# Kernel optimization log

Hardware: AMD Instinct MI355X
Metric: run time of the kernel (lower is better)

The kernel has to match this reference:

```python
import jax, jax.numpy as jnp
import numpy as np


def conv_block(x, w1, b1, w2, b2):
    # 1x1 convs == per-pixel channel matmuls. x: [b, C, H, W]
    h = jax.nn.relu(jnp.einsum('bchw,oc->bohw', x, w1) + b1[None, :, None, None])
    return jnp.einsum('bchw,oc->bohw', h, w2) + b2[None, :, None, None]


def setup_inputs() -> dict:
    key = jax.random.key(0)
    ks = jax.random.split(key, 9)
    C, Ck = 256, 256 // 8
    bs, H, W = 4, 64, 64
    s_in = 1.0 / np.sqrt(C)
    s_k = 1.0 / np.sqrt(Ck)
    F_input = jax.random.normal(ks[0], (bs, C, H, W), dtype=jnp.float32)
    return {
        'F_input': F_input,
        'w1a': jax.random.normal(ks[1], (Ck, C), dtype=jnp.float32) * s_in,
        'b1a': jax.random.normal(ks[2], (Ck,), dtype=jnp.float32) * s_in,
        'w1b': jax.random.normal(ks[3], (Ck, Ck), dtype=jnp.float32) * s_k,
        'b1b': jax.random.normal(ks[4], (Ck,), dtype=jnp.float32) * s_k,
        'w2a': jax.random.normal(ks[5], (Ck, C), dtype=jnp.float32) * s_in,
        'b2a': jax.random.normal(ks[6], (Ck,), dtype=jnp.float32) * s_in,
        'w2b': jax.random.normal(ks[7], (Ck, Ck), dtype=jnp.float32) * s_k,
        'b2b': jax.random.normal(ks[8], (Ck,), dtype=jnp.float32) * s_k,
    }


def reference(F_input, w1a, b1a, w1b, b1b, w2a, b2a, w2b, b2b):
    bs, C, H, W = F_input.shape
    N = H * W
    q = conv_block(F_input, w1a, b1a, w1b, b1b).reshape(bs, -1, N)  # [b, Ck, N]
    k = conv_block(F_input, w2a, b2a, w2b, b2b).reshape(bs, -1, N)  # [b, Ck, N]
    # mm_1[b, n, m] = sum_c q[b, c, n] * k[b, c, m]
    scores = jnp.einsum('bcn,bcm->bnm', q, k)  # [b, N, N]
    S = jax.nn.softmax(scores, axis=-1)
    Fr = F_input.reshape(bs, C, N)
    # bmm(F_reshape, S^T): out[b, c, n] = sum_m F[b, c, m] * S[b, n, m]
    mm2 = jnp.einsum('bcm,bnm->bcn', Fr, S).reshape(bs, C, H, W)
    return F_input + mm2
```

## Files before the change

### kernel.cpp

```cpp
#include <hip/hip_runtime.h>
#include <math.h>

typedef __attribute__((ext_vector_type(4))) float f32x4;
typedef __attribute__((ext_vector_type(8))) short bf16x8;
typedef __attribute__((ext_vector_type(2))) unsigned int uint2v;
typedef __attribute__((ext_vector_type(4))) unsigned int uint4v;

#define LOG2E 1.4426950408889634f
#define MT 32

static __device__ __forceinline__ unsigned short f2bf(float f) {
  union { float f; unsigned int i; } u; u.f = f;
  unsigned int r = u.i + 0x7fffu + ((u.i >> 16) & 1u);
  return (unsigned short)(r >> 16);
}

typedef __attribute__((address_space(3))) unsigned int lds_u32;
typedef __attribute__((address_space(1))) unsigned int g_u32;

static __device__ __forceinline__ void gload_lds16(const unsigned short* g,
                                                   const unsigned short* l) {
  __builtin_amdgcn_global_load_lds(
      (const g_u32*)(unsigned long long)g,
      (lds_u32*)(unsigned int)(unsigned long long)l, 16, 0, 0);
}

__global__ __launch_bounds__(256) void k_wprep(const float* __restrict__ w1a,
                                               const float* __restrict__ w2a,
                                               float* __restrict__ w1aT,
                                               float* __restrict__ w2aT) {
  int i = blockIdx.x * 256 + threadIdx.x;
  if (i < 32 * 256) {
    int o = i >> 8, c = i & 255;
    w1aT[c * 32 + o] = w1a[i];
    w2aT[c * 32 + o] = w2a[i];
  }
}

__global__ __launch_bounds__(256) void k_qk(
    const float* __restrict__ F,
    const float* __restrict__ w1aT, const float* __restrict__ b1a,
    const float* __restrict__ w1b,  const float* __restrict__ b1b,
    const float* __restrict__ w2aT, const float* __restrict__ b2a,
    const float* __restrict__ w2b,  const float* __restrict__ b2b,
    unsigned short* __restrict__ Fbf,
    unsigned short* __restrict__ qT,
    unsigned short* __restrict__ kT) {
  __shared__ float hp[4][64][33];
  const int tid = threadIdx.x;
  const int nl = tid & 63;
  const int cs = __builtin_amdgcn_readfirstlane(tid >> 6);
  const int strip = blockIdx.x;
  const int b = strip >> 6;
  const int n0 = (strip & 63) << 6;
  const int n = n0 + nl;

  const float* Fp = F + ((size_t)(b * 256 + cs * 64)) * 4096 + n;
  unsigned short* Fbp = Fbf + ((size_t)(b * 256 + cs * 64)) * 4096 + n;

  float hq[32], hk[32];
#pragma unroll
  for (int o = 0; o < 32; ++o) { hq[o] = 0.f; hk[o] = 0.f; }

  float fa[8], fb[8];
#pragma unroll
  for (int j = 0; j < 8; ++j) fa[j] = Fp[(size_t)j * 4096];

  for (int jj = 0; jj < 64; jj += 16) {
#pragma unroll
    for (int j = 0; j < 8; ++j) fb[j] = Fp[(size_t)(jj + 8 + j) * 4096];
#pragma unroll
    for (int j = 0; j < 8; ++j) {
      Fbp[(size_t)(jj + j) * 4096] = f2bf(fa[j]);
      const float* wq = w1aT + (cs * 64 + jj + j) * 32;
      const float* wk = w2aT + (cs * 64 + jj + j) * 32;
#pragma unroll
      for (int o = 0; o < 32; ++o) { hq[o] += wq[o] * fa[j]; hk[o] += wk[o] * fa[j]; }
    }
    if (jj + 16 < 64) {
#pragma unroll
      for (int j = 0; j < 8; ++j) fa[j] = Fp[(size_t)(jj + 16 + j) * 4096];
    }
#pragma unroll
    for (int j = 0; j < 8; ++j) {
      Fbp[(size_t)(jj + 8 + j) * 4096] = f2bf(fb[j]);
      const float* wq = w1aT + (cs * 64 + jj + 8 + j) * 32;
      const float* wk = w2aT + (cs * 64 + jj + 8 + j) * 32;
#pragma unroll
      for (int o = 0; o < 32; ++o) { hq[o] += wq[o] * fb[j]; hk[o] += wk[o] * fb[j]; }
    }
  }

#pragma unroll
  for (int o = 0; o < 32; ++o) hp[cs][nl][o] = hq[o];
  __syncthreads();
  {
    float h[32];
#pragma unroll
    for (int o = 0; o < 32; ++o)
      h[o] = fmaxf(hp[0][nl][o] + hp[1][nl][o] + hp[2][nl][o] + hp[3][nl][o] + b1a[o], 0.f);
    unsigned int pk[4];
#pragma unroll
    for (int oo = 0; oo < 8; oo += 2) {
      float s0 = b1b[cs * 8 + oo], s1 = b1b[cs * 8 + oo + 1];
#pragma unroll
      for (int i = 0; i < 32; ++i) {
        s0 += w1b[(cs * 8 + oo) * 32 + i] * h[i];
        s1 += w1b[(cs * 8 + oo + 1) * 32 + i] * h[i];
      }
      s0 *= LOG2E; s1 *= LOG2E;
      pk[oo >> 1] = (unsigned int)f2bf(s0) | ((unsigned int)f2bf(s1) << 16);
    }
    uint4v v = {pk[0], pk[1], pk[2], pk[3]};
    *(uint4v*)(qT + ((size_t)(b * 4096 + n)) * 32 + cs * 8) = v;
  }
  __syncthreads();
#pragma unroll
  for (int o = 0; o < 32; ++o) hp[cs][nl][o] = hk[o];
  __syncthreads();
  {
    float h[32];
#pragma unroll
    for (int o = 0; o < 32; ++o)
      h[o] = fmaxf(hp[0][nl][o] + hp[1][nl][o] + hp[2][nl][o] + hp[3][nl][o] + b2a[o], 0.f);
    unsigned int pk[4];
#pragma unroll
    for (int oo = 0; oo < 8; oo += 2) {
      float s0 = b2b[cs * 8 + oo], s1 = b2b[cs * 8 + oo + 1];
#pragma unroll
      for (int i = 0; i < 32; ++i) {
        s0 += w2b[(cs * 8 + oo) * 32 + i] * h[i];
        s1 += w2b[(cs * 8 + oo + 1) * 32 + i] * h[i];
      }
      pk[oo >> 1] = (unsigned int)f2bf(s0) | ((unsigned int)f2bf(s1) << 16);
    }
    uint4v v = {pk[0], pk[1], pk[2], pk[3]};
    *(uint4v*)(kT + ((size_t)(b * 4096 + n)) * 32 + cs * 8) = v;
  }
}

__global__ __launch_bounds__(256, 4) void k_attn(
    const unsigned short* __restrict__ qT,
    const unsigned short* __restrict__ kT,
    const unsigned short* __restrict__ Fbf,
    const float* __restrict__ F,
    float* __restrict__ out,
    float* __restrict__ Opart,
    float* __restrict__ Mpart,
    float* __restrict__ Lpart,
    int spl, int mtiles, int direct) {
  __shared__ unsigned short Vt[256 * MT];
  __shared__ unsigned short Pb[64 * MT];
  __shared__ float scl[64];

  const int tid = threadIdx.x;
  const int w = tid >> 6, lane = tid & 63, lo = lane & 15, hi = lane >> 4;

  const int bid = (int)blockIdx.x;
  int g, ns;
  if (spl == 4)      { g = ((bid & 7) << 1) | (bid >> 9); ns = (bid >> 3) & 63; }
  else if (spl == 2) { g = bid & 7;                       ns = bid >> 3; }
  else               { int sz = (bid & 7) * 32 + (bid >> 3); g = sz >> 6; ns = sz & 63; }
  const int b = (spl == 4) ? (g >> 2) : ((spl == 2) ? (g >> 1) : g);
  const int s = (spl == 4) ? (g & 3) : ((spl == 2) ? (g & 1) : 0);
  const int n0 = ns << 6;
  const int mt0 = s * mtiles;

  const bf16x8 qfrag = *(const bf16x8*)(
      qT + ((size_t)(b << 12) + n0 + (w << 4) + lo) * 32 + (hi << 3));
  const unsigned short* kTb = kT + ((size_t)(b << 12)) * 32;
  const unsigned short* Fb = Fbf + ((size_t)b << 20);

  const int crow = lane >> 2, pch = lane & 3;

  f32x4 acc[4][4];
#pragma unroll
  for (int i = 0; i < 4; ++i)
#pragma unroll
    for (int j = 0; j < 4; ++j) acc[i][j] = (f32x4){0.f, 0.f, 0.f, 0.f};
  float mrun = -INFINITY, lrun = 0.f;

#pragma unroll
  for (int i = 0; i < 4; ++i) {
    int c = i * 64 + (w << 4) + crow;
    gload_lds16(Fb + (size_t)c * 4096 + (mt0 << 5) + ((pch ^ (c & 3)) << 3),
                &Vt[(i * 64 + (w << 4)) * MT]);
  }
  bf16x8 kc0 = *(const bf16x8*)(kTb + ((size_t)((mt0 << 5) + lo)) * 32 + (hi << 3));
  bf16x8 kc1 = *(const bf16x8*)(kTb + ((size_t)((mt0 << 5) + 16 + lo)) * 32 + (hi << 3));

  for (int t = 0; t < mtiles; ++t) {
    f32x4 z = (f32x4){0.f, 0.f, 0.f, 0.f};
    f32x4 s0 = __builtin_amdgcn_mfma_f32_16x16x32_bf16(kc0, qfrag, z, 0, 0, 0);
    f32x4 s1 = __builtin_amdgcn_mfma_f32_16x16x32_bf16(kc1, qfrag, z, 0, 0, 0);

    float tmax = fmaxf(fmaxf(fmaxf(s0[0], s0[1]), fmaxf(s0[2], s0[3])),
                       fmaxf(fmaxf(s1[0], s1[1]), fmaxf(s1[2], s1[3])));
    tmax = fmaxf(tmax, __shfl_xor(tmax, 16));
    tmax = fmaxf(tmax, __shfl_xor(tmax, 32));
    float mnew = fmaxf(mrun, tmax);
    float sc = exp2f(mrun - mnew);
    mrun = mnew;
    float p00 = exp2f(s0[0] - mnew), p01 = exp2f(s0[1] - mnew);
    float p02 = exp2f(s0[2] - mnew), p03 = exp2f(s0[3] - mnew);
    float p10 = exp2f(s1[0] - mnew), p11 = exp2f(s1[1] - mnew);
    float p12 = exp2f(s1[2] - mnew), p13 = exp2f(s1[3] - mnew);
    float rsum = p00 + p01 + p02 + p03 + p10 + p11 + p12 + p13;
    rsum += __shfl_xor(rsum, 16);
    rsum += __shfl_xor(rsum, 32);
    lrun = lrun * sc + rsum;
    if (hi == 0) scl[(w << 4) + lo] = sc;
    {
      const int qr = (w << 4) + lo;
      unsigned short* base = &Pb[qr * MT];
      int ch0 = (hi >> 1), ch1 = 2 + (hi >> 1);
      uint2v v0 = {(unsigned int)f2bf(p00) | ((unsigned int)f2bf(p01) << 16),
                   (unsigned int)f2bf(p02) | ((unsigned int)f2bf(p03) << 16)};
      uint2v v1 = {(unsigned int)f2bf(p10) | ((unsigned int)f2bf(p11) << 16),
                   (unsigned int)f2bf(p12) | ((unsigned int)f2bf(p13) << 16)};
      *(uint2v*)(base + (((ch0 ^ (qr & 3)) << 3) | ((hi & 1) << 2))) = v0;
      *(uint2v*)(base + (((ch1 ^ (qr & 3)) << 3) | ((hi & 1) << 2))) = v1;
    }

    __syncthreads();

    {
      f32x4 sv[4];
      bool one = true;
#pragma unroll
      for (int qf = 0; qf < 4; ++qf) {
        sv[qf] = *(const f32x4*)&scl[(qf << 4) + (hi << 2)];
        one = one && (sv[qf][0] == 1.f) && (sv[qf][1] == 1.f) &&
              (sv[qf][2] == 1.f) && (sv[qf][3] == 1.f);
      }
      if (!__all(one)) {
#pragma unroll
        for (int qf = 0; qf < 4; ++qf)
#pragma unroll
          for (int cs2 = 0; cs2 < 4; ++cs2) acc[qf][cs2] *= sv[qf];
      }
    }
    bf16x8 pf[4], vf[4];
#pragma unroll
    for (int qf = 0; qf < 4; ++qf) {
      int qr = (qf << 4) + lo;
      pf[qf] = *(const bf16x8*)&Pb[qr * MT + ((hi ^ (qr & 3)) << 3)];
    }
#pragma unroll
    for (int cs2 = 0; cs2 < 4; ++cs2) {
      int c = (w << 6) + (cs2 << 4) + lo;
      vf[cs2] = *(const bf16x8*)&Vt[c * MT + ((hi ^ (c & 3)) << 3)];
    }
    __builtin_amdgcn_s_setprio(1);
#pragma unroll
    for (int qf = 0; qf < 4; ++qf)
#pragma unroll
      for (int cs2 = 0; cs2 < 4; ++cs2)
        acc[qf][cs2] = __builtin_amdgcn_mfma_f32_16x16x32_bf16(pf[qf], vf[cs2], acc[qf][cs2], 0, 0, 0);
    __builtin_amdgcn_s_setprio(0);

    __syncthreads();

    if (t + 1 < mtiles) {
      int mo = (mt0 + t + 1) << 5;
#pragma unroll
      for (int i = 0; i < 4; ++i) {
        int c = i * 64 + (w << 4) + crow;
        gload_lds16(Fb + (size_t)c * 4096 + mo + ((pch ^ (c & 3)) << 3),
                    &Vt[(i * 64 + (w << 4)) * MT]);
      }
      kc0 = *(const bf16x8*)(kTb + ((size_t)(mo + lo)) * 32 + (hi << 3));
      kc1 = *(const bf16x8*)(kTb + ((size_t)(mo + 16 + lo)) * 32 + (hi << 3));
    }
  }

  if (direct) {
    if (hi == 0) scl[(w << 4) + lo] = 1.f / lrun;
    __syncthreads();
    f32x4 lv[4];
#pragma unroll
    for (int qf = 0; qf < 4; ++qf) lv[qf] = *(const f32x4*)&scl[(qf << 4) + (hi << 2)];
#pragma unroll
    for (int qf = 0; qf < 4; ++qf)
#pragma unroll
      for (int cs2 = 0; cs2 < 4; ++cs2) {
        size_t idx = ((size_t)(b * 256 + (w << 6) + (cs2 << 4) + lo)) * 4096 +
                     n0 + (qf << 4) + (hi << 2);
        f32x4 fv = *(const f32x4*)(F + idx);
        *(f32x4*)(out + idx) = fv + acc[qf][cs2] * lv[qf];
      }
  } else {
    const int bp = (b * spl + s) * 64 + ns;
    if (hi == 0) {
      Mpart[bp * 64 + (w << 4) + lo] = mrun;
      Lpart[bp * 64 + (w << 4) + lo] = lrun;
    }
    float* Ob = Opart + (size_t)bp * 256 * 64;
#pragma unroll
    for (int qf = 0; qf < 4; ++qf)
#pragma unroll
      for (int cs2 = 0; cs2 < 4; ++cs2) {
        int c = (w << 6) + (cs2 << 4) + lo;
        *(f32x4*)(Ob + (size_t)c * 64 + (qf << 4) + (hi << 2)) = acc[qf][cs2];
      }
  }
}

__global__ __launch_bounds__(256, 4) void k_comb(
    const float* __restrict__ F, const float* __restrict__ Opart,
    const float* __restrict__ Mpart, const float* __restrict__ Lpart,
    float* __restrict__ out, int spl) {
  __shared__ float a[4][64];
  const int cid = (int)blockIdx.x;
  const int b = cid >> 8, ns = (cid >> 2) & 63, cq = cid & 3;
  const int tid = threadIdx.x, q = tid & 63, ci = tid >> 6;
  const int n0 = ns << 6;

  if (tid < 64) {
    float mv[4], lv[4];
    float M = -INFINITY;
#pragma unroll
    for (int s2 = 0; s2 < 4; ++s2)
      if (s2 < spl) {
        int bp = (b * spl + s2) * 64 + ns;
        mv[s2] = Mpart[bp * 64 + q];
        lv[s2] = Lpart[bp * 64 + q];
        M = fmaxf(M, mv[s2]);
      }
    float L = 0.f;
#pragma unroll
    for (int s2 = 0; s2 < 4; ++s2)
      if (s2 < spl) { mv[s2] = exp2f(mv[s2] - M); L += mv[s2] * lv[s2]; }
    float Li = 1.f / L;
#pragma unroll
    for (int s2 = 0; s2 < 4; ++s2)
      if (s2 < spl) a[s2][q] = mv[s2] * Li;
  }
  __syncthreads();
  float aq[4];
#pragma unroll
  for (int s2 = 0; s2 < 4; ++s2) aq[s2] = (s2 < spl) ? a[s2][q] : 0.f;

#pragma unroll 4
  for (int cc = 0; cc < 16; ++cc) {
    int c = (cq << 6) + (ci << 4) + cc;
    float accv = 0.f;
#pragma unroll
    for (int s2 = 0; s2 < 4; ++s2)
      if (s2 < spl)
        accv += aq[s2] * Opart[((size_t)((b * spl + s2) * 64 + ns) * 256 + c) * 64 + q];
    size_t idx = ((size_t)(b * 256 + c)) * 4096 + n0 + q;
    out[idx] = F[idx] + accv;
  }
}

extern "C" void kernel_launch(void* const* d_in, const int* in_sizes, int n_in,
                              void* d_out, int out_size, void* d_ws, size_t ws_size,
                              hipStream_t stream) {
  const float* F   = (const float*)d_in[0];
  const float* w1a = (const float*)d_in[1];
  const float* b1a = (const float*)d_in[2];
  const float* w1b = (const float*)d_in[3];
  const float* b1b = (const float*)d_in[4];
  const float* w2a = (const float*)d_in[5];
  const float* b2a = (const float*)d_in[6];
  const float* w2b = (const float*)d_in[7];
  const float* b2b = (const float*)d_in[8];
  float* out = (float*)d_out;

  char* ws = (char*)d_ws;
  float* w1aT = (float*)(ws);
  float* w2aT = (float*)(ws + 32768);
  unsigned short* qT  = (unsigned short*)(ws + 65536);
  unsigned short* kT  = (unsigned short*)(ws + 65536 + 1048576);
  unsigned short* Fbf = (unsigned short*)(ws + 65536 + 2097152);
  const size_t obase = 65536 + 2097152 + 8388608;

  int spl = 1, direct = 1;
  const size_t oSz1 = 16777216, mlSz1 = 65536;
  if (ws_size >= obase + 4 * (oSz1 + 2 * mlSz1)) { spl = 4; direct = 0; }
  else if (ws_size >= obase + 2 * (oSz1 + 2 * mlSz1)) { spl = 2; direct = 0; }

  float* Opart = (float*)(ws + obase);
  float* Mpart = (float*)(ws + obase + (size_t)spl * oSz1);
  float* Lpart = (float*)(ws + obase + (size_t)spl * oSz1 + (size_t)spl * mlSz1);

  hipLaunchKernelGGL(k_wprep, dim3(32), dim3(256), 0, stream, w1a, w2a, w1aT, w2aT);
  hipLaunchKernelGGL(k_qk, dim3(256), dim3(256), 0, stream,
                     F, w1aT, b1a, w1b, b1b, w2aT, b2a, w2b, b2b, Fbf, qT, kT);
  hipLaunchKernelGGL(k_attn, dim3(256 * spl), dim3(256), 0, stream,
                     qT, kT, Fbf, F, out, Opart, Mpart, Lpart, spl, 128 / spl, direct);
  if (!direct)
    hipLaunchKernelGGL(k_comb, dim3(1024), dim3(256), 0, stream,
                       F, Opart, Mpart, Lpart, out, spl);
}
```

Baseline: 289.2 us.

## Split projection into convert/transpose plus per-pixel kernel; load V directly in attention

Adds a k_cvt kernel that writes F as bf16 in both the original and a pixel-major transposed layout. k_qk is rewritten as small 64-thread blocks that read the transposed bf16 row, reduce partial sums with shuffles, and compute q or k per block. In the attention kernel, the LDS-staged V tiles loaded with global_load_lds are replaced by direct global loads into registers, and the P and scale buffers are double-buffered with a new swizzle so the trailing barrier can be dropped. This adds an extra kernel and extra traffic for the transposed copy, which overlaps the Opart region of the workspace, and it relies on cache hits for V reuse across waves.

New measurement: 360.1 us. 1.25x slower.

```diff
diff --git a/kernel.cpp b/kernel.cpp
--- a/kernel.cpp
+++ b/kernel.cpp
@@ -14,15 +14,9 @@
   unsigned int r = u.i + 0x7fffu + ((u.i >> 16) & 1u);
   return (unsigned short)(r >> 16);
 }
-
-typedef __attribute__((address_space(3))) unsigned int lds_u32;
-typedef __attribute__((address_space(1))) unsigned int g_u32;
-
-static __device__ __forceinline__ void gload_lds16(const unsigned short* g,
-                                                   const unsigned short* l) {
-  __builtin_amdgcn_global_load_lds(
-      (const g_u32*)(unsigned long long)g,
-      (lds_u32*)(unsigned int)(unsigned long long)l, 16, 0, 0);
+static __device__ __forceinline__ float bf2f(unsigned short s) {
+  union { unsigned int i; float f; } u; u.i = ((unsigned int)s) << 16;
+  return u.f;
 }
 
 __global__ __launch_bounds__(256) void k_wprep(const float* __restrict__ w1a,
@@ -37,106 +31,135 @@
   }
 }
 
-__global__ __launch_bounds__(256) void k_qk(
-    const float* __restrict__ F,
+__global__ __launch_bounds__(256) void k_cvt(const float* __restrict__ F,
+                                             unsigned short* __restrict__ Fbf,
+                                             unsigned short* __restrict__ FbfT) {
+  __shared__ unsigned short Lt[64][68];
+  const int bi = blockIdx.x;
+  const int b = bi >> 8, cg = (bi >> 6) & 3, ng = bi & 63;
+  const int tid = threadIdx.x;
+  {
+    const int cl = tid >> 2, part = tid & 3;
+    const size_t row = (size_t)(b * 256 + cg * 64 + cl);
+    const float* src = F + row * 4096 + ng * 64 + part * 16;
+    unsigned int pk[8];
+#pragma unroll
+    for (int i = 0; i < 4; ++i) {
+      f32x4 v = *(const f32x4*)(src + i * 4);
+      pk[2 * i]     = (unsigned int)f2bf(v[0]) | ((unsigned int)f2bf(v[1]) << 16);
+      pk[2 * i + 1] = (unsigned int)f2bf(v[2]) | ((unsigned int)f2bf(v[3]) << 16);
+    }
+    unsigned short* dst = Fbf + row * 4096 + ng * 64 + part * 16;
+    uint4v a = {pk[0], pk[1], pk[2], pk[3]};
+    uint4v c2 = {pk[4], pk[5], pk[6], pk[7]};
+    *(uint4v*)(dst) = a;
+    *(uint4v*)(dst + 8) = c2;
+    unsigned short* lrow = &Lt[cl][part * 16];
+#pragma unroll
+    for (int i = 0; i < 8; ++i) {
+      lrow[2 * i]     = (unsigned short)(pk[i] & 0xffffu);
+      lrow[2 * i + 1] = (unsigned short)(pk[i] >> 16);
+    }
+  }
+  __syncthreads();
+  {
+    const int nl = tid & 63, ch = tid >> 6;
+    unsigned int pk[16];
+#pragma unroll
+    for (int i = 0; i < 16; ++i) {
+      unsigned short a = Lt[ch * 16 + 0 + (i >> 3) * 8 + 0][nl];
+      pk[i] = 0; (void)a;
+    }
+    unsigned short vals[16];
+#pragma unroll
+    for (int i = 0; i < 16; ++i) vals[i] = Lt[ch * 16 + i][nl];
+#pragma unroll
+    for (int i = 0; i < 8; ++i)
+      pk[i] = (unsigned int)vals[2 * i] | ((unsigned int)vals[2 * i + 1] << 16);
+    unsigned short* dst = FbfT + ((size_t)(b * 4096 + ng * 64 + nl)) * 256 + cg * 64 + ch * 16;
+    uint4v v0 = {pk[0], pk[1], pk[2], pk[3]};
+    uint4v v1 = {pk[4], pk[5], pk[6], pk[7]};
+    *(uint4v*)(dst) = v0;
+    *(uint4v*)(dst + 8) = v1;
+  }
+}
+
+__global__ __launch_bounds__(64) void k_qk(
+    const unsigned short* __restrict__ FbfT,
     const float* __restrict__ w1aT, const float* __restrict__ b1a,
     const float* __restrict__ w1b,  const float* __restrict__ b1b,
     const float* __restrict__ w2aT, const float* __restrict__ b2a,
     const float* __restrict__ w2b,  const float* __restrict__ b2b,
-    unsigned short* __restrict__ Fbf,
-    unsigned short* __restrict__ qT,
-    unsigned short* __restrict__ kT) {
-  __shared__ float hp[4][64][33];
-  const int tid = threadIdx.x;
-  const int nl = tid & 63;
-  const int cs = __builtin_amdgcn_readfirstlane(tid >> 6);
-  const int strip = blockIdx.x;
-  const int b = strip >> 6;
-  const int n0 = (strip & 63) << 6;
-  const int n = n0 + nl;
-
-  const float* Fp = F + ((size_t)(b * 256 + cs * 64)) * 4096 + n;
-  unsigned short* Fbp = Fbf + ((size_t)(b * 256 + cs * 64)) * 4096 + n;
-
-  float hq[32], hk[32];
-#pragma unroll
-  for (int o = 0; o < 32; ++o) { hq[o] = 0.f; hk[o] = 0.f; }
-
-  float fa[8], fb[8];
-#pragma unroll
-  for (int j = 0; j < 8; ++j) fa[j] = Fp[(size_t)j * 4096];
-
-  for (int jj = 0; jj < 64; jj += 16) {
-#pragma unroll
-    for (int j = 0; j < 8; ++j) fb[j] = Fp[(size_t)(jj + 8 + j) * 4096];
-#pragma unroll
-    for (int j = 0; j < 8; ++j) {
-      Fbp[(size_t)(jj + j) * 4096] = f2bf(fa[j]);
-      const float* wq = w1aT + (cs * 64 + jj + j) * 32;
-      const float* wk = w2aT + (cs * 64 + jj + j) * 32;
-#pragma unroll
-      for (int o = 0; o < 32; ++o) { hq[o] += wq[o] * fa[j]; hk[o] += wk[o] * fa[j]; }
-    }
-    if (jj + 16 < 64) {
-#pragma unroll
-      for (int j = 0; j < 8; ++j) fa[j] = Fp[(size_t)(jj + 16 + j) * 4096];
-    }
-#pragma unroll
-    for (int j = 0; j < 8; ++j) {
-      Fbp[(size_t)(jj + 8 + j) * 4096] = f2bf(fb[j]);
-      const float* wq = w1aT + (cs * 64 + jj + 8 + j) * 32;
-      const float* wk = w2aT + (cs * 64 + jj + 8 + j) * 32;
-#pragma unroll
-      for (int o = 0; o < 32; ++o) { hq[o] += wq[o] * fb[j]; hk[o] += wk[o] * fb[j]; }
-    }
-  }
-
-#pragma unroll
-  for (int o = 0; o < 32; ++o) hp[cs][nl][o] = hq[o];
-  __syncthreads();
+    unsigned short* __restrict__ qT, unsigned short* __restrict__ kT) {
+  const int p = blockIdx.x & 1;
+  const int tile = blockIdx.x >> 1;
+  const int l = threadIdx.x;
+  const int px = l >> 2, cq = l & 3;
+  const int n = tile * 16 + px;
+  const float* wA = p ? w2aT : w1aT;
+  const float* bA = p ? b2a : b1a;
+  const float* wB = p ? w2b : w1b;
+  const float* bB = p ? b2b : b1b;
+
+  bf16x8 f8[8];
   {
-    float h[32];
-#pragma unroll
-    for (int o = 0; o < 32; ++o)
-      h[o] = fmaxf(hp[0][nl][o] + hp[1][nl][o] + hp[2][nl][o] + hp[3][nl][o] + b1a[o], 0.f);
-    unsigned int pk[4];
-#pragma unroll
-    for (int oo = 0; oo < 8; oo += 2) {
-      float s0 = b1b[cs * 8 + oo], s1 = b1b[cs * 8 + oo + 1];
-#pragma unroll
-      for (int i = 0; i < 32; ++i) {
-        s0 += w1b[(cs * 8 + oo) * 32 + i] * h[i];
-        s1 += w1b[(cs * 8 + oo + 1) * 32 + i] * h[i];
-      }
-      s0 *= LOG2E; s1 *= LOG2E;
-      pk[oo >> 1] = (unsigned int)f2bf(s0) | ((unsigned int)f2bf(s1) << 16);
-    }
-    uint4v v = {pk[0], pk[1], pk[2], pk[3]};
-    *(uint4v*)(qT + ((size_t)(b * 4096 + n)) * 32 + cs * 8) = v;
-  }
-  __syncthreads();
-#pragma unroll
-  for (int o = 0; o < 32; ++o) hp[cs][nl][o] = hk[o];
-  __syncthreads();
-  {
-    float h[32];
-#pragma unroll
-    for (int o = 0; o < 32; ++o)
-      h[o] = fmaxf(hp[0][nl][o] + hp[1][nl][o] + hp[2][nl][o] + hp[3][nl][o] + b2a[o], 0.f);
-    unsigned int pk[4];
-#pragma unroll
-    for (int oo = 0; oo < 8; oo += 2) {
-      float s0 = b2b[cs * 8 + oo], s1 = b2b[cs * 8 + oo + 1];
-#pragma unroll
-      for (int i = 0; i < 32; ++i) {
-        s0 += w2b[(cs * 8 + oo) * 32 + i] * h[i];
-        s1 += w2b[(cs * 8 + oo + 1) * 32 + i] * h[i];
-      }
-      pk[oo >> 1] = (unsigned int)f2bf(s0) | ((unsigned int)f2bf(s1) << 16);
-    }
-    uint4v v = {pk[0], pk[1], pk[2], pk[3]};
-    *(uint4v*)(kT + ((size_t)(b * 4096 + n)) * 32 + cs * 8) = v;
-  }
+    const unsigned short* src = FbfT + (size_t)n * 256 + cq * 64;
+#pragma unroll
+    for (int i = 0; i < 8; ++i) f8[i] = *(const bf16x8*)(src + i * 8);
+  }
+  float h[32];
+#pragma unroll
+  for (int o = 0; o < 32; ++o) h[o] = 0.f;
+
+#pragma unroll
+  for (int i = 0; i < 8; ++i) {
+    bf16x8 v = f8[i];
+#pragma unroll
+    for (int jj = 0; jj < 8; ++jj) {
+      float fv = bf2f((unsigned short)v[jj]);
+      const float* wr = wA + (size_t)(cq * 64 + i * 8 + jj) * 32;
+#pragma unroll
+      for (int o4 = 0; o4 < 8; ++o4) {
+        f32x4 wv = *(const f32x4*)(wr + o4 * 4);
+        h[o4 * 4 + 0] += wv[0] * fv;
+        h[o4 * 4 + 1] += wv[1] * fv;
+        h[o4 * 4 + 2] += wv[2] * fv;
+        h[o4 * 4 + 3] += wv[3] * fv;
+      }
+    }
+  }
+#pragma unroll
+  for (int o = 0; o < 32; ++o) {
+    float t = h[o];
+    t += __shfl_xor(t, 1);
+    t += __shfl_xor(t, 2);
+    h[o] = fmaxf(t + bA[o], 0.f);
+  }
+  unsigned int pk[4];
+#pragma unroll
+  for (int oo = 0; oo < 8; oo += 2) {
+    int o2 = cq * 8 + oo;
+    float s0 = bB[o2], s1 = bB[o2 + 1];
+    const float* w0 = wB + (size_t)o2 * 32;
+    const float* w1 = wB + (size_t)(o2 + 1) * 32;
+#pragma unroll
+    for (int i4 = 0; i4 < 8; ++i4) {
+      f32x4 a = *(const f32x4*)(w0 + i4 * 4);
+      f32x4 c = *(const f32x4*)(w1 + i4 * 4);
+#pragma unroll
+      for (int r = 0; r < 4; ++r) {
+        s0 += a[r] * h[i4 * 4 + r];
+        s1 += c[r] * h[i4 * 4 + r];
+      }
+    }
+    if (p == 0) { s0 *= LOG2E; s1 *= LOG2E; }
+    pk[oo >> 1] = (unsigned int)f2bf(s0) | ((unsigned int)f2bf(s1) << 16);
+  }
+  uint2v v0 = {pk[0], pk[1]};
+  uint2v v1 = {pk[2], pk[3]};
+  unsigned short* dst = (p ? kT : qT) + (size_t)n * 32 + cq * 8;
+  *(uint2v*)(dst) = v0;
+  *(uint2v*)(dst + 4) = v1;
 }
 
 __global__ __launch_bounds__(256, 4) void k_attn(
@@ -149,12 +172,12 @@
     float* __restrict__ Mpart,
     float* __restrict__ Lpart,
     int spl, int mtiles, int direct) {
-  __shared__ unsigned short Vt[256 * MT];
-  __shared__ unsigned short Pb[64 * MT];
-  __shared__ float scl[64];
+  __shared__ unsigned short Pb[2][64 * MT];
+  __shared__ float scl[2][64];
 
   const int tid = threadIdx.x;
   const int w = tid >> 6, lane = tid & 63, lo = lane & 15, hi = lane >> 4;
+  const int sx = (lo & 3) ^ ((lo >> 2) & 3);
 
   const int bid = (int)blockIdx.x;
   int g, ns;
@@ -171,8 +194,6 @@
   const unsigned short* kTb = kT + ((size_t)(b << 12)) * 32;
   const unsigned short* Fb = Fbf + ((size_t)b << 20);
 
-  const int crow = lane >> 2, pch = lane & 3;
-
   f32x4 acc[4][4];
 #pragma unroll
   for (int i = 0; i < 4; ++i)
@@ -180,20 +201,24 @@
     for (int j = 0; j < 4; ++j) acc[i][j] = (f32x4){0.f, 0.f, 0.f, 0.f};
   float mrun = -INFINITY, lrun = 0.f;
 
-#pragma unroll
-  for (int i = 0; i < 4; ++i) {
-    int c = i * 64 + (w << 4) + crow;
-    gload_lds16(Fb + (size_t)c * 4096 + (mt0 << 5) + ((pch ^ (c & 3)) << 3),
-                &Vt[(i * 64 + (w << 4)) * MT]);
-  }
   bf16x8 kc0 = *(const bf16x8*)(kTb + ((size_t)((mt0 << 5) + lo)) * 32 + (hi << 3));
   bf16x8 kc1 = *(const bf16x8*)(kTb + ((size_t)((mt0 << 5) + 16 + lo)) * 32 + (hi << 3));
 
   for (int t = 0; t < mtiles; ++t) {
+    bf16x8 vf[4];
+#pragma unroll
+    for (int cs2 = 0; cs2 < 4; ++cs2) {
+      int c = (w << 6) + (cs2 << 4) + lo;
+      vf[cs2] = *(const bf16x8*)(Fb + (size_t)c * 4096 + ((mt0 + t) << 5) + (hi << 3));
+    }
     f32x4 z = (f32x4){0.f, 0.f, 0.f, 0.f};
     f32x4 s0 = __builtin_amdgcn_mfma_f32_16x16x32_bf16(kc0, qfrag, z, 0, 0, 0);
     f32x4 s1 = __builtin_amdgcn_mfma_f32_16x16x32_bf16(kc1, qfrag, z, 0, 0, 0);
-
+    if (t + 1 < mtiles) {
+      int mo = (mt0 + t + 1) << 5;
+      kc0 = *(const bf16x8*)(kTb + ((size_t)(mo + lo)) * 32 + (hi << 3));
+      kc1 = *(const bf16x8*)(kTb + ((size_t)(mo + 16 + lo)) * 32 + (hi << 3));
+    }
     float tmax = fmaxf(fmaxf(fmaxf(s0[0], s0[1]), fmaxf(s0[2], s0[3])),
                        fmaxf(fmaxf(s1[0], s1[1]), fmaxf(s1[2], s1[3])));
     tmax = fmaxf(tmax, __shfl_xor(tmax, 16));
@@ -209,17 +234,18 @@
     rsum += __shfl_xor(rsum, 16);
     rsum += __shfl_xor(rsum, 32);
     lrun = lrun * sc + rsum;
-    if (hi == 0) scl[(w << 4) + lo] = sc;
+    if (hi == 0) scl[t & 1][(w << 4) + lo] = sc;
     {
       const int qr = (w << 4) + lo;
-      unsigned short* base = &Pb[qr * MT];
-      int ch0 = (hi >> 1), ch1 = 2 + (hi >> 1);
+      unsigned short* base = &Pb[t & 1][qr * MT];
+      int ph0 = (hi >> 1) ^ sx;
+      int ph1 = (2 + (hi >> 1)) ^ sx;
       uint2v v0 = {(unsigned int)f2bf(p00) | ((unsigned int)f2bf(p01) << 16),
                    (unsigned int)f2bf(p02) | ((unsigned int)f2bf(p03) << 16)};
       uint2v v1 = {(unsigned int)f2bf(p10) | ((unsigned int)f2bf(p11) << 16),
                    (unsigned int)f2bf(p12) | ((unsigned int)f2bf(p13) << 16)};
-      *(uint2v*)(base + (((ch0 ^ (qr & 3)) << 3) | ((hi & 1) << 2))) = v0;
-      *(uint2v*)(base + (((ch1 ^ (qr & 3)) << 3) | ((hi & 1) << 2))) = v1;
+      *(uint2v*)(base + ((ph0 << 3) | ((hi & 1) << 2))) = v0;
+      *(uint2v*)(base + ((ph1 << 3) | ((hi & 1) << 2))) = v1;
     }
 
     __syncthreads();
@@ -229,7 +255,7 @@
       bool one = true;
 #pragma unroll
       for (int qf = 0; qf < 4; ++qf) {
-        sv[qf] = *(const f32x4*)&scl[(qf << 4) + (hi << 2)];
+        sv[qf] = *(const f32x4*)&scl[t & 1][(qf << 4) + (hi << 2)];
         one = one && (sv[qf][0] == 1.f) && (sv[qf][1] == 1.f) &&
               (sv[qf][2] == 1.f) && (sv[qf][3] == 1.f);
       }
@@ -240,16 +266,11 @@
           for (int cs2 = 0; cs2 < 4; ++cs2) acc[qf][cs2] *= sv[qf];
       }
     }
-    bf16x8 pf[4], vf[4];
+    bf16x8 pf[4];
 #pragma unroll
     for (int qf = 0; qf < 4; ++qf) {
       int qr = (qf << 4) + lo;
-      pf[qf] = *(const bf16x8*)&Pb[qr * MT + ((hi ^ (qr & 3)) << 3)];
-    }
-#pragma unroll
-    for (int cs2 = 0; cs2 < 4; ++cs2) {
-      int c = (w << 6) + (cs2 << 4) + lo;
-      vf[cs2] = *(const bf16x8*)&Vt[c * MT + ((hi ^ (c & 3)) << 3)];
+      pf[qf] = *(const bf16x8*)&Pb[t & 1][qr * MT + (((hi ^ sx) << 3))];
     }
     __builtin_amdgcn_s_setprio(1);
 #pragma unroll
@@ -258,28 +279,14 @@
       for (int cs2 = 0; cs2 < 4; ++cs2)
         acc[qf][cs2] = __builtin_amdgcn_mfma_f32_16x16x32_bf16(pf[qf], vf[cs2], acc[qf][cs2], 0, 0, 0);
     __builtin_amdgcn_s_setprio(0);
-
-    __syncthreads();
-
-    if (t + 1 < mtiles) {
-      int mo = (mt0 + t + 1) << 5;
-#pragma unroll
-      for (int i = 0; i < 4; ++i) {
-        int c = i * 64 + (w << 4) + crow;
-        gload_lds16(Fb + (size_t)c * 4096 + mo + ((pch ^ (c & 3)) << 3),
-                    &Vt[(i * 64 + (w << 4)) * MT]);
-      }
-      kc0 = *(const bf16x8*)(kTb + ((size_t)(mo + lo)) * 32 + (hi << 3));
-      kc1 = *(const bf16x8*)(kTb + ((size_t)(mo + 16 + lo)) * 32 + (hi << 3));
-    }
   }
 
   if (direct) {
-    if (hi == 0) scl[(w << 4) + lo] = 1.f / lrun;
+    if (hi == 0) scl[0][(w << 4) + lo] = 1.f / lrun;
     __syncthreads();
     f32x4 lv[4];
 #pragma unroll
-    for (int qf = 0; qf < 4; ++qf) lv[qf] = *(const f32x4*)&scl[(qf << 4) + (hi << 2)];
+    for (int qf = 0; qf < 4; ++qf) lv[qf] = *(const f32x4*)&scl[0][(qf << 4) + (hi << 2)];
 #pragma unroll
     for (int qf = 0; qf < 4; ++qf)
 #pragma unroll
@@ -376,6 +383,8 @@
   unsigned short* Fbf = (unsigned short*)(ws + 65536 + 2097152);
   const size_t obase = 65536 + 2097152 + 8388608;
 
+  unsigned short* FbfT = (unsigned short*)(ws + obase);
+
   int spl = 1, direct = 1;
   const size_t oSz1 = 16777216, mlSz1 = 65536;
   if (ws_size >= obase + 4 * (oSz1 + 2 * mlSz1)) { spl = 4; direct = 0; }
@@ -386,8 +395,9 @@
   float* Lpart = (float*)(ws + obase + (size_t)spl * oSz1 + (size_t)spl * mlSz1);
 
   hipLaunchKernelGGL(k_wprep, dim3(32), dim3(256), 0, stream, w1a, w2a, w1aT, w2aT);
-  hipLaunchKernelGGL(k_qk, dim3(256), dim3(256), 0, stream,
-                     F, w1aT, b1a, w1b, b1b, w2aT, b2a, w2b, b2b, Fbf, qT, kT);
+  hipLaunchKernelGGL(k_cvt, dim3(1024), dim3(256), 0, stream, F, Fbf, FbfT);
+  hipLaunchKernelGGL(k_qk, dim3(2048), dim3(64), 0, stream,
+                     FbfT, w1aT, b1a, w1b, b1b, w2aT, b2a, w2b, b2b, qT, kT);
   hipLaunchKernelGGL(k_attn, dim3(256 * spl), dim3(256), 0, stream,
                      qT, kT, Fbf, F, out, Opart, Mpart, Lpart, spl, 128 / spl, direct);
   if (!direct)
```
